# Kernel tuning notes

Hardware: AMD Instinct MI355X
Metric: run time of the kernel (lower is better)

Reference implementation:

```python
import jax, jax.numpy as jnp
import numpy as np

ALPHA = 0.2  # LeakyReLU negative slope
NEG_INF = -1.0e12


def setup_inputs() -> dict:
    key = jax.random.key(0)
    k1, k2, k3, k4 = jax.random.split(key, 4)
    B, N, Fin, Fout = 4, 4096, 256, 128
    inp = jax.random.normal(k1, (B, N, Fin), dtype=jnp.float32)
    adj_weights = jax.random.uniform(k2, (B, N, N), dtype=jnp.float32)
    W = jax.random.normal(k3, (Fin, Fout), dtype=jnp.float32) * (1.414 / np.sqrt(Fin))
    a = jax.random.normal(k4, (2 * Fout, 1), dtype=jnp.float32) * 0.1
    return {"inp": inp, "adj_weights": adj_weights, "W": W, "a": a}


def reference(inp, adj_weights, W, a):
    Fout = W.shape[1]
    h = jnp.matmul(inp, W)                       # [B, N, Fout]
    # a_input[b,i,j] = concat(h[b,i], h[b,j]); matmul with a splits into two rank-1 terms
    a1 = a[:Fout, 0]                             # [Fout]
    a2 = a[Fout:, 0]                             # [Fout]
    s1 = jnp.einsum('bnf,f->bn', h, a1)          # [B, N]
    s2 = jnp.einsum('bnf,f->bn', h, a2)          # [B, N]
    e = jax.nn.leaky_relu(s1[:, :, None] + s2[:, None, :], negative_slope=ALPHA)  # [B,N,N]
    attention = jnp.where(adj_weights > 0, adj_weights * e, NEG_INF)
    attention = jax.nn.softmax(attention, axis=2)
    # dropout p=0.0 / eval mode -> identity
    h_prime = jnp.matmul(attention, h)           # [B, N, Fout]
    return jax.nn.elu(h_prime)                   # concat=True branch
```

## Files before the change

### kernel.cpp

```cpp
#include <hip/hip_runtime.h>
#include <math.h>

typedef float    float4_t __attribute__((ext_vector_type(4)));
typedef _Float16 half8    __attribute__((ext_vector_type(8)));
typedef _Float16 half4_t  __attribute__((ext_vector_type(4)));

__global__ __launch_bounds__(256) void k_prep(const float* __restrict__ inp,
                                              const float* __restrict__ W,
                                              const float* __restrict__ a,
                                              float* __restrict__ s1,
                                              float* __restrict__ s2,
                                              _Float16* __restrict__ hT) {
    __shared__ float sA[32 * 68];
    __shared__ float sW[64 * 128];
    const int t   = threadIdx.x;
    const int gr0 = blockIdx.x * 32;
    const int b   = gr0 >> 12;
    const int f0  = (t & 15) * 8;
    const int r0  = (t >> 4) * 2;
    float4_t acc0[2] = {}; float4_t acc1[2] = {};
    for (int kc = 0; kc < 4; ++kc) {
        __syncthreads();
        #pragma unroll
        for (int it = 0; it < 2; ++it) {
            int fi = it * 256 + t; int r = fi >> 4; int c = (fi & 15) * 4;
            *(float4_t*)&sA[r * 68 + c] =
                *(const float4_t*)&inp[(size_t)(gr0 + r) * 256 + kc * 64 + c];
        }
        #pragma unroll
        for (int it = 0; it < 8; ++it) {
            int fi = it * 256 + t; int k = fi >> 5; int c = (fi & 31) * 4;
            *(float4_t*)&sW[k * 128 + c] =
                *(const float4_t*)&W[(size_t)(kc * 64 + k) * 128 + c];
        }
        __syncthreads();
        for (int k = 0; k < 64; ++k) {
            float4_t w0 = *(const float4_t*)&sW[k * 128 + f0];
            float4_t w1 = *(const float4_t*)&sW[k * 128 + f0 + 4];
            #pragma unroll
            for (int r = 0; r < 2; ++r) {
                float av = sA[(r0 + r) * 68 + k];
                acc0[r] += av * w0; acc1[r] += av * w1;
            }
        }
    }
    float4_t a1lo = *(const float4_t*)&a[f0];
    float4_t a1hi = *(const float4_t*)&a[f0 + 4];
    float4_t a2lo = *(const float4_t*)&a[128 + f0];
    float4_t a2hi = *(const float4_t*)&a[128 + f0 + 4];
    #pragma unroll
    for (int r = 0; r < 2; ++r) {
        const int row  = gr0 + r0 + r;
        const int rloc = row & 4095;
        #pragma unroll
        for (int c = 0; c < 4; ++c) {
            hT[(size_t)b * (128 * 4096) + (size_t)(f0 + c) * 4096 + rloc]     = (_Float16)acc0[r][c];
            hT[(size_t)b * (128 * 4096) + (size_t)(f0 + 4 + c) * 4096 + rloc] = (_Float16)acc1[r][c];
        }
        float p1 = acc0[r][0]*a1lo[0] + acc0[r][1]*a1lo[1] + acc0[r][2]*a1lo[2] + acc0[r][3]*a1lo[3]
                 + acc1[r][0]*a1hi[0] + acc1[r][1]*a1hi[1] + acc1[r][2]*a1hi[2] + acc1[r][3]*a1hi[3];
        float p2 = acc0[r][0]*a2lo[0] + acc0[r][1]*a2lo[1] + acc0[r][2]*a2lo[2] + acc0[r][3]*a2lo[3]
                 + acc1[r][0]*a2hi[0] + acc1[r][1]*a2hi[1] + acc1[r][2]*a2hi[2] + acc1[r][3]*a2hi[3];
        #pragma unroll
        for (int o = 1; o < 16; o <<= 1) { p1 += __shfl_xor(p1, o); p2 += __shfl_xor(p2, o); }
        if ((t & 15) == 0) { s1[row] = p1; s2[row] = p2; }
    }
}

__global__ __launch_bounds__(256) void k_s2max(const float* __restrict__ s2,
                                               float* __restrict__ s2max) {
    const int b = blockIdx.x, t = threadIdx.x;
    float m = -INFINITY;
    for (int i = t; i < 4096; i += 256) m = fmaxf(m, s2[b * 4096 + i]);
    #pragma unroll
    for (int o = 1; o < 64; o <<= 1) m = fmaxf(m, __shfl_xor(m, o));
    __shared__ float sm[4];
    if ((t & 63) == 0) sm[t >> 6] = m;
    __syncthreads();
    if (t == 0) s2max[b] = fmaxf(fmaxf(sm[0], sm[1]), fmaxf(sm[2], sm[3]));
}

__global__ __launch_bounds__(256, 4) void k_flash(const float* __restrict__ adj,
                                                  const _Float16* __restrict__ hT,
                                                  const float* __restrict__ s1,
                                                  const float* __restrict__ s2,
                                                  const float* __restrict__ s2max,
                                                  float* __restrict__ part_acc,
                                                  float* __restrict__ part_l) {
    __shared__ _Float16 pbuf[4][16 * 64];

    const int t    = threadIdx.x;
    const int bid  = blockIdx.x;
    const int sp   = bid & 3;
    const int rb   = (bid >> 2) & 63;
    const int b    = bid >> 8;
    const int w    = t >> 6, lane = t & 63;
    const int quad = lane >> 4, ln15 = lane & 15;
    const int g    = quad;
    const int cl   = ln15;
    const int rowb = rb * 64 + w * 16;
    const float*    adj_w = adj + (size_t)b * 4096 * 4096 + (size_t)rowb * 4096;
    const _Float16* hT_b  = hT + (size_t)b * 128 * 4096;
    const float*    s2_b  = s2 + b * 4096;
    const float     s2m   = s2max[b];
    const int jwbase = sp * 1024;

    float s1r[4], mh[4];
    #pragma unroll
    for (int L = 0; L < 4; ++L) {
        s1r[L] = s1[b * 4096 + rowb + L * 4 + g];
        mh[L]  = fmaxf(0.f, s1r[L] + s2m);
    }

    const _Float16* hT_lane = hT_b + (size_t)ln15 * 4096 + (quad << 3);

    float4_t acc[8] = {};
    float4_t psacc = {0.f, 0.f, 0.f, 0.f};

    float4_t av[4];
    float4_t s2v;
    #pragma unroll
    for (int L = 0; L < 4; ++L)
        av[L] = *(const float4_t*)&adj_w[(size_t)(L * 4 + g) * 4096 + jwbase + cl * 4];
    s2v = *(const float4_t*)&s2_b[jwbase + cl * 4];

    for (int jt = 0; jt < 16; ++jt) {
        const int j0 = jwbase + jt * 64;
        #pragma unroll
        for (int L = 0; L < 4; ++L) {
            half4_t qv;
            #pragma unroll
            for (int c = 0; c < 4; ++c) {
                float x = s1r[L] + s2v[c];
                float e = x > 0.f ? x : 0.2f * x;
                float p = av[L][c] > 0.f ? __expf(fmaf(av[L][c], e, -mh[L])) : 0.f;
                _Float16 q = (_Float16)p;
                qv[c] = q;
                psacc[L] += (float)q;
            }
            const int r     = L * 4 + g;
            const int c0    = cl * 4;
            const int chunk = (c0 >> 3) ^ (r & 7);
            *(half4_t*)&pbuf[w][r * 64 + chunk * 8 + (c0 & 7)] = qv;
        }
        if (jt < 15) {
            #pragma unroll
            for (int L = 0; L < 4; ++L)
                av[L] = *(const float4_t*)&adj_w[(size_t)(L * 4 + g) * 4096 + j0 + 64 + cl * 4];
            s2v = *(const float4_t*)&s2_b[j0 + 64 + cl * 4];
        }
        half8 bf[2][2];
        bf[0][0] = *(const half8*)&hT_lane[j0];
        bf[0][1] = *(const half8*)&hT_lane[j0 + 32];
        asm volatile("s_waitcnt lgkmcnt(0)" ::: "memory");
        half8 afrag[2];
        #pragma unroll
        for (int kc = 0; kc < 2; ++kc) {
            const int chunk = ((kc << 2) + quad) ^ (ln15 & 7);
            afrag[kc] = *(const half8*)&pbuf[w][ln15 * 64 + chunk * 8];
        }
        #pragma unroll
        for (int nt = 0; nt < 8; ++nt) {
            const int cb = nt & 1;
            if (nt < 7) {
                bf[cb ^ 1][0] = *(const half8*)&hT_lane[(size_t)(nt + 1) * 16 * 4096 + j0];
                bf[cb ^ 1][1] = *(const half8*)&hT_lane[(size_t)(nt + 1) * 16 * 4096 + j0 + 32];
            }
            acc[nt] = __builtin_amdgcn_mfma_f32_16x16x32_f16(afrag[0], bf[cb][0], acc[nt], 0, 0, 0);
            acc[nt] = __builtin_amdgcn_mfma_f32_16x16x32_f16(afrag[1], bf[cb][1], acc[nt], 0, 0, 0);
        }
    }
    #pragma unroll
    for (int o = 1; o < 16; o <<= 1) {
        #pragma unroll
        for (int L = 0; L < 4; ++L) psacc[L] += __shfl_xor(psacc[L], o);
    }
    const size_t growb = (size_t)b * 4096 + rowb;
    if (cl == 0) {
        #pragma unroll
        for (int L = 0; L < 4; ++L)
            part_l[(size_t)sp * 16384 + growb + L * 4 + g] = psacc[L];
    }
    float* pacc = part_acc + (size_t)sp * 16384 * 128;
    #pragma unroll
    for (int nt = 0; nt < 8; ++nt) {
        #pragma unroll
        for (int reg = 0; reg < 4; ++reg) {
            pacc[(growb + quad * 4 + reg) * 128 + nt * 16 + ln15] = acc[nt][reg];
        }
    }
}

__global__ __launch_bounds__(256) void k_combine(const float* __restrict__ part_acc,
                                                 const float* __restrict__ part_l,
                                                 float* __restrict__ out) {
    const int idx = blockIdx.x * 256 + threadIdx.x;
    const int e0  = idx * 4;
    const int gr  = e0 >> 7;
    float l = part_l[gr] + part_l[16384 + gr] + part_l[32768 + gr] + part_l[49152 + gr];
    float4_t a0 = *(const float4_t*)&part_acc[e0];
    float4_t a1 = *(const float4_t*)&part_acc[2097152 + e0];
    float4_t a2 = *(const float4_t*)&part_acc[4194304 + e0];
    float4_t a3 = *(const float4_t*)&part_acc[6291456 + e0];
    float4_t s  = (a0 + a1) + (a2 + a3);
    float rl = 1.f / l;
    float4_t o;
    #pragma unroll
    for (int c = 0; c < 4; ++c) {
        float v = s[c] * rl;
        o[c] = v > 0.f ? v : expm1f(v);
    }
    *(float4_t*)&((float*)out)[e0] = o;
}

extern "C" void kernel_launch(void* const* d_in, const int* in_sizes, int n_in,
                              void* d_out, int out_size, void* d_ws, size_t ws_size,
                              hipStream_t stream) {
    const float* inp = (const float*)d_in[0];
    const float* adj = (const float*)d_in[1];
    const float* W   = (const float*)d_in[2];
    const float* a   = (const float*)d_in[3];
    float* out = (float*)d_out;

    char* wsb = (char*)d_ws;
    _Float16* hT       = (_Float16*)(wsb);
    float*    s1       = (float*)(wsb + 4194304);
    float*    s2       = (float*)(wsb + 4259840);
    float*    s2max    = (float*)(wsb + 4325376);
    float*    part_l   = (float*)(wsb + 4325632);
    float*    part_acc = (float*)(wsb + 4587776);

    hipLaunchKernelGGL(k_prep,    dim3(512),  dim3(256), 0, stream, inp, W, a, s1, s2, hT);
    hipLaunchKernelGGL(k_s2max,   dim3(4),    dim3(256), 0, stream, s2, s2max);
    hipLaunchKernelGGL(k_flash,   dim3(1024), dim3(256), 0, stream, adj, hT, s1, s2, s2max,
                       part_acc, part_l);
    hipLaunchKernelGGL(k_combine, dim3(2048), dim3(256), 0, stream, part_acc, part_l, out);
}
```

Baseline: 476.7 us.

## Stage hT tiles in shared memory across 16 waves per block

The flash kernel now runs 1024-thread blocks covering 256 rows each. Each block cooperatively loads 256-column chunks of hT into swizzled LDS, and all 16 waves read their MFMA B fragments from there instead of each wave loading hT from global memory itself. The aim is to cut redundant global/L2 traffic for hT, but it adds block-wide barriers and grows LDS use to 96KB per block. With only 256 blocks of 1024 threads, occupancy and latency hiding for the adj stream may drop. The staging store also contains a stray scalar write that is immediately overwritten by the vector store.

```diff
diff --git a/kernel.cpp b/kernel.cpp
--- a/kernel.cpp
+++ b/kernel.cpp
@@ -80,25 +80,26 @@
     if (t == 0) s2max[b] = fmaxf(fmaxf(sm[0], sm[1]), fmaxf(sm[2], sm[3]));
 }
 
-__global__ __launch_bounds__(256, 4) void k_flash(const float* __restrict__ adj,
-                                                  const _Float16* __restrict__ hT,
-                                                  const float* __restrict__ s1,
-                                                  const float* __restrict__ s2,
-                                                  const float* __restrict__ s2max,
-                                                  float* __restrict__ part_acc,
-                                                  float* __restrict__ part_l) {
-    __shared__ _Float16 pbuf[4][16 * 64];
+__global__ __launch_bounds__(1024) void k_flash(const float* __restrict__ adj,
+                                                const _Float16* __restrict__ hT,
+                                                const float* __restrict__ s1,
+                                                const float* __restrict__ s2,
+                                                const float* __restrict__ s2max,
+                                                float* __restrict__ part_acc,
+                                                float* __restrict__ part_l) {
+    __shared__ _Float16 hbuf[4 * 128 * 64];
+    __shared__ _Float16 pbuf[16][16 * 64];
 
     const int t    = threadIdx.x;
     const int bid  = blockIdx.x;
     const int sp   = bid & 3;
-    const int rb   = (bid >> 2) & 63;
-    const int b    = bid >> 8;
+    const int rbb  = (bid >> 2) & 15;
+    const int b    = bid >> 6;
     const int w    = t >> 6, lane = t & 63;
     const int quad = lane >> 4, ln15 = lane & 15;
     const int g    = quad;
     const int cl   = ln15;
-    const int rowb = rb * 64 + w * 16;
+    const int rowb = rbb * 256 + w * 16;
     const float*    adj_w = adj + (size_t)b * 4096 * 4096 + (size_t)rowb * 4096;
     const _Float16* hT_b  = hT + (size_t)b * 128 * 4096;
     const float*    s2_b  = s2 + b * 4096;
@@ -112,64 +113,82 @@
         mh[L]  = fmaxf(0.f, s1r[L] + s2m);
     }
 
-    const _Float16* hT_lane = hT_b + (size_t)ln15 * 4096 + (quad << 3);
+    const int sf  = t >> 3;
+    const int sc  = t & 7;
+    const int fb7 = ln15 & 7;
 
     float4_t acc[8] = {};
     float4_t psacc = {0.f, 0.f, 0.f, 0.f};
-
     float4_t av[4];
     float4_t s2v;
+
     #pragma unroll
     for (int L = 0; L < 4; ++L)
         av[L] = *(const float4_t*)&adj_w[(size_t)(L * 4 + g) * 4096 + jwbase + cl * 4];
     s2v = *(const float4_t*)&s2_b[jwbase + cl * 4];
 
-    for (int jt = 0; jt < 16; ++jt) {
-        const int j0 = jwbase + jt * 64;
-        #pragma unroll
-        for (int L = 0; L < 4; ++L) {
-            half4_t qv;
-            #pragma unroll
-            for (int c = 0; c < 4; ++c) {
-                float x = s1r[L] + s2v[c];
-                float e = x > 0.f ? x : 0.2f * x;
-                float p = av[L][c] > 0.f ? __expf(fmaf(av[L][c], e, -mh[L])) : 0.f;
-                _Float16 q = (_Float16)p;
-                qv[c] = q;
-                psacc[L] += (float)q;
-            }
-            const int r     = L * 4 + g;
-            const int c0    = cl * 4;
-            const int chunk = (c0 >> 3) ^ (r & 7);
-            *(half4_t*)&pbuf[w][r * 64 + chunk * 8 + (c0 & 7)] = qv;
-        }
-        if (jt < 15) {
-            #pragma unroll
-            for (int L = 0; L < 4; ++L)
-                av[L] = *(const float4_t*)&adj_w[(size_t)(L * 4 + g) * 4096 + j0 + 64 + cl * 4];
-            s2v = *(const float4_t*)&s2_b[j0 + 64 + cl * 4];
-        }
-        half8 bf[2][2];
-        bf[0][0] = *(const half8*)&hT_lane[j0];
-        bf[0][1] = *(const half8*)&hT_lane[j0 + 32];
-        asm volatile("s_waitcnt lgkmcnt(0)" ::: "memory");
-        half8 afrag[2];
-        #pragma unroll
-        for (int kc = 0; kc < 2; ++kc) {
-            const int chunk = ((kc << 2) + quad) ^ (ln15 & 7);
-            afrag[kc] = *(const half8*)&pbuf[w][ln15 * 64 + chunk * 8];
-        }
-        #pragma unroll
-        for (int nt = 0; nt < 8; ++nt) {
-            const int cb = nt & 1;
-            if (nt < 7) {
-                bf[cb ^ 1][0] = *(const half8*)&hT_lane[(size_t)(nt + 1) * 16 * 4096 + j0];
-                bf[cb ^ 1][1] = *(const half8*)&hT_lane[(size_t)(nt + 1) * 16 * 4096 + j0 + 32];
-            }
-            acc[nt] = __builtin_amdgcn_mfma_f32_16x16x32_f16(afrag[0], bf[cb][0], acc[nt], 0, 0, 0);
-            acc[nt] = __builtin_amdgcn_mfma_f32_16x16x32_f16(afrag[1], bf[cb][1], acc[nt], 0, 0, 0);
-        }
-    }
+    #pragma unroll 1
+    for (int st = 0; st < 4; ++st) {
+        if (st) __syncthreads();
+        {
+            const int stb = jwbase + st * 256;
+            half8 hreg[4];
+            #pragma unroll
+            for (int i = 0; i < 4; ++i)
+                hreg[i] = *(const half8*)&hT_b[(size_t)sf * 4096 + stb + i * 64 + sc * 8];
+            #pragma unroll
+            for (int i = 0; i < 4; ++i)
+                hbuf[(i * 128 + sf) * 64 + ((sc ^ (sf & 7)) << 3)] = hreg[i][0],
+                *(half8*)&hbuf[(i * 128 + sf) * 64 + ((sc ^ (sf & 7)) << 3)] = hreg[i];
+        }
+        __syncthreads();
+        #pragma unroll
+        for (int q = 0; q < 4; ++q) {
+            const int it = st * 4 + q;
+            const int j0 = jwbase + it * 64;
+            #pragma unroll
+            for (int L = 0; L < 4; ++L) {
+                half4_t qv;
+                #pragma unroll
+                for (int c = 0; c < 4; ++c) {
+                    float x = s1r[L] + s2v[c];
+                    float e = x > 0.f ? x : 0.2f * x;
+                    float p = av[L][c] > 0.f ? __expf(fmaf(av[L][c], e, -mh[L])) : 0.f;
+                    _Float16 qq = (_Float16)p;
+                    qv[c] = qq;
+                    psacc[L] += (float)qq;
+                }
+                const int r     = L * 4 + g;
+                const int c0    = cl * 4;
+                const int chunk = (c0 >> 3) ^ (r & 7);
+                *(half4_t*)&pbuf[w][r * 64 + chunk * 8 + (c0 & 7)] = qv;
+            }
+            if (it < 15) {
+                #pragma unroll
+                for (int L = 0; L < 4; ++L)
+                    av[L] = *(const float4_t*)&adj_w[(size_t)(L * 4 + g) * 4096 + j0 + 64 + cl * 4];
+                s2v = *(const float4_t*)&s2_b[j0 + 64 + cl * 4];
+            }
+            asm volatile("s_waitcnt lgkmcnt(0)" ::: "memory");
+            half8 afrag[2];
+            #pragma unroll
+            for (int kc = 0; kc < 2; ++kc) {
+                const int chunk = ((kc << 2) + quad) ^ (ln15 & 7);
+                afrag[kc] = *(const half8*)&pbuf[w][ln15 * 64 + chunk * 8];
+            }
+            const _Float16* hsub = &hbuf[q * 128 * 64];
+            #pragma unroll
+            for (int nt = 0; nt < 8; ++nt) {
+                #pragma unroll
+                for (int kc = 0; kc < 2; ++kc) {
+                    const int fb = nt * 16 + ln15;
+                    half8 bfrag = *(const half8*)&hsub[fb * 64 + ((((kc << 2) + quad) ^ fb7) << 3)];
+                    acc[nt] = __builtin_amdgcn_mfma_f32_16x16x32_f16(afrag[kc], bfrag, acc[nt], 0, 0, 0);
+                }
+            }
+        }
+    }
+
     #pragma unroll
     for (int o = 1; o < 16; o <<= 1) {
         #pragma unroll
@@ -232,7 +251,7 @@
 
     hipLaunchKernelGGL(k_prep,    dim3(512),  dim3(256), 0, stream, inp, W, a, s1, s2, hT);
     hipLaunchKernelGGL(k_s2max,   dim3(4),    dim3(256), 0, stream, s2, s2max);
-    hipLaunchKernelGGL(k_flash,   dim3(1024), dim3(256), 0, stream, adj, hT, s1, s2, s2max,
+    hipLaunchKernelGGL(k_flash,   dim3(256),  dim3(1024), 0, stream, adj, hT, s1, s2, s2max,
                        part_acc, part_l);
     hipLaunchKernelGGL(k_combine, dim3(2048), dim3(256), 0, stream, part_acc, part_l, out);
 }
```

Result: no change. 477.7 us (+0.2%).
